# Kernel optimization log

Measured on AMD Instinct MI355X. Metric: run time of the kernel, lower is better.

The kernel has to match this reference:

```python
import jax, jax.numpy as jnp
import numpy as np

B, T, HS, WS = 4, 16, 32, 64          # batch, time, lat, lon
D_MODEL, N_HEADS = 256, 8
E = D_MODEL // N_HEADS                 # 32 per-head dim
MODES = [8, 8, 16]
F_LAST = WS // 2 + 1                   # 33 rfft bins on last dim
M_LAST = MODES[-1]                     # 16 kept rfft bins
M_PANEL = MODES[0] * MODES[1]          # 64 kept (T,HS) panel modes


def _sym_indexes(shape):
    # faithful numpy port of get_symmetry_index_in_fft_pannel
    shape = np.array(shape)
    idx = np.stack([t.flatten() for t in np.meshgrid(*[range(s) for s in shape])])
    idx2 = (-idx) % shape[:, None]
    fftshift = (idx + shape[:, None] // 2) % shape[:, None]
    center = (shape[:, None] - 1) / 2
    order = np.argsort(np.linalg.norm(fftshift - center, axis=0))
    idx = idx[:, order]
    idx2 = idx2[:, order]
    return np.ravel_multi_index(idx, shape), np.ravel_multi_index(idx2, shape)


def _picked_panel():
    # lowest-frequency mode selection honoring Hermitian pairing
    i1, i2 = _sym_indexes((T, HS))
    picked = []
    for a, b in zip(i1, i2):
        if a in picked or b in picked:
            continue
        picked.append(a)
        if len(picked) == M_PANEL:
            break
    return np.array(picked, dtype=np.int32), i1.astype(np.int32), i2.astype(np.int32)


def setup_inputs() -> dict:
    key = jax.random.key(0)
    ks = jax.random.split(key, 12)
    sl = 1.0 / np.float32(np.sqrt(D_MODEL))
    sw = np.float32(0.02)
    panel, s1, s2 = _picked_panel()
    return {
        "x": jax.random.normal(ks[0], (B, T, HS, WS, D_MODEL), jnp.float32),
        "Wq": jax.random.normal(ks[1], (D_MODEL, D_MODEL), jnp.float32) * sl,
        "bq": jnp.zeros((D_MODEL,), jnp.float32),
        "Wk": jax.random.normal(ks[2], (D_MODEL, D_MODEL), jnp.float32) * sl,
        "bk": jnp.zeros((D_MODEL,), jnp.float32),
        "Wv": jax.random.normal(ks[3], (D_MODEL, D_MODEL), jnp.float32) * sl,
        "bv": jnp.zeros((D_MODEL,), jnp.float32),
        "Wo": jax.random.normal(ks[4], (D_MODEL, D_MODEL), jnp.float32) * sl,
        "bo": jnp.zeros((D_MODEL,), jnp.float32),
        "w_real": jax.random.normal(ks[5], (N_HEADS, E, E, M_PANEL, M_LAST), jnp.float32) * sw,
        "w_imag": jax.random.normal(ks[6], (N_HEADS, E, E, M_PANEL, M_LAST), jnp.float32) * sw,
        "panel_idx": jnp.asarray(panel),
        "sym_idx1": jnp.asarray(s1),
        "sym_idx2": jnp.asarray(s2),
    }


def reference(x, Wq, bq, Wk, bk, Wv, bv, Wo, bo, w_real, w_imag,
              panel_idx, sym_idx1, sym_idx2):
    # QKV projections (the torch layer computes all three; FourierBlockN uses q)
    q = (x @ Wq + bq).reshape(B, T, HS, WS, N_HEADS, E).transpose(0, 4, 5, 1, 2, 3)
    _k = (x @ Wk + bk)
    _v = (x @ Wv + bv)
    # rfftn over the spacetime dims -> (B,H,E,T,HS,F_LAST)
    x_ft = jnp.fft.rfftn(q, axes=(-3, -2, -1)).reshape(B, N_HEADS, E, T * HS, F_LAST)
    # gather selected frequency modes
    x_sel = x_ft[:, :, :, panel_idx, :M_LAST]                    # (B,H,E,Mp,Ml)
    w = w_real + 1j * w_imag                                      # (H,E,E,Mp,Ml)
    out_sel = jnp.einsum('bhipf,hiopf->bhopf', x_sel, w)
    out_ft = jnp.zeros_like(x_ft)
    out_ft = out_ft.at[:, :, :, panel_idx, :M_LAST].set(out_sel)
    # canonical_fft_freq: enforce Hermitian symmetry on the (T,HS) panel
    out_ft = out_ft.at[:, :, :, sym_idx1, :].set(
        (out_ft[:, :, :, sym_idx1, :] + jnp.conj(out_ft[:, :, :, sym_idx2, :])) * 0.5)
    out_ft = out_ft.reshape(B, N_HEADS, E, T, HS, F_LAST)
    o = jnp.fft.irfftn(out_ft, s=(T, HS, WS), axes=(-3, -2, -1))  # (B,H,E,T,HS,WS)
    o = o.transpose(0, 3, 4, 5, 1, 2).reshape(B, T, HS, WS, N_HEADS * E)
    return o @ Wo + bo
```

## Files before the change

kernel.cpp:

```cpp
#include <hip/hip_runtime.h>
#include <hip/hip_bf16.h>
#include <cmath>

#define BB 4
#define TT 16
#define HH 32
#define WW 64
#define DD 256
#define NHEAD 8
#define EE 32
#define MP 64
#define ML 16
#define SPAT 32768
#define S2D 512

constexpr size_t OFF_FTRE = 0;
constexpr size_t OFF_FTIM = 1024;
constexpr size_t OFF_FHRE = 2048;
constexpr size_t OFF_FHIM = 4096;
constexpr size_t OFF_CW   = 6144;
constexpr size_t OFF_W64I = 7168;
constexpr size_t OFF_W16  = 9216;
constexpr size_t OFF_FHT  = 9728;
constexpr size_t OFF_GB   = 16384;
constexpr size_t OFF_FW   = OFF_GB + 8388608;
constexpr size_t OFF_X    = OFF_FW + 16777216;
constexpr size_t OFF_V    = OFF_X + 2097152;
constexpr size_t OFF_WT   = OFF_V + 2097152;

typedef short short8 __attribute__((ext_vector_type(8)));
typedef float f32x4 __attribute__((ext_vector_type(4)));

static __device__ __forceinline__ unsigned short f2bf(float x) {
  union { float f; unsigned u; } v; v.f = x;
  unsigned r = v.u + 0x7fffu + ((v.u >> 16) & 1u);
  return (unsigned short)(r >> 16);
}

static __device__ __forceinline__ void gl_lds16(const void* g, void* l) {
  __builtin_amdgcn_global_load_lds((const __attribute__((address_space(1))) void*)g,
                                   (__attribute__((address_space(3))) void*)l, 16, 0, 0);
}

__global__ __launch_bounds__(256) void k0_tables(const int* __restrict__ panel, float* __restrict__ tab) {
  __shared__ int kt[MP], kh[MP];
  int tid = threadIdx.x;
  if (tid < MP) { int s = panel[tid]; kt[tid] = s >> 5; kh[tid] = s & 31; }
  __syncthreads();
  const double PI2 = 6.283185307179586476925286766559;
  for (int i = tid; i < 1024; i += 256) {
    int p = i >> 4, t = i & 15;
    double a = -PI2 * (double)((t * kt[p]) & 15) / 16.0;
    tab[OFF_FTRE + i] = (float)cos(a);
    tab[OFF_FTIM + i] = (float)sin(a);
  }
  for (int i = tid; i < 2048; i += 256) {
    int p = i >> 5, hs = i & 31;
    double a = -PI2 * (double)((hs * kh[p]) & 31) / 32.0;
    tab[OFF_FHRE + i] = (float)cos(a);
    tab[OFF_FHIM + i] = (float)sin(a);
  }
  for (int i = tid; i < 1024; i += 256) {
    int f = i >> 6, wsx = i & 63;
    double a = PI2 * (double)((f * wsx) & 63) / 64.0;
    tab[OFF_CW + i] = (f == 0) ? (1.0f / 64.0f) : (float)(2.0 * cos(a) / 64.0);
  }
  for (int i = tid; i < 2048; i += 256) {
    int wsx = i >> 5, f2 = i & 31; int f = f2 >> 1;
    double a = -PI2 * (double)((wsx * f) & 63) / 64.0;
    tab[OFF_W64I + i] = (f2 & 1) ? (float)sin(a) : (float)cos(a);
  }
  if (tid < 256) {
    int t = tid >> 4, k = tid & 15;
    double a = -PI2 * (double)((t * k) & 15) / 16.0;
    tab[OFF_W16 + 2 * tid]     = (float)cos(a);
    tab[OFF_W16 + 2 * tid + 1] = (float)sin(a);
  }
  for (int i = tid; i < 2048; i += 256) {
    int hs = i >> 6, p = i & 63;
    double a = -PI2 * (double)((hs * kh[p]) & 31) / 32.0;
    tab[OFF_FHT + 2 * i]     = (float)cos(a);
    tab[OFF_FHT + 2 * i + 1] = (float)sin(a);
  }
}

__global__ __launch_bounds__(256) void conv_w(const float* __restrict__ Wq, const float* __restrict__ Wo,
                                              unsigned short* __restrict__ wqt, unsigned short* __restrict__ wot) {
  __shared__ float tile[32][33];
  const float* src = blockIdx.z ? Wo : Wq;
  unsigned short* dst = blockIdx.z ? wot : wqt;
  int k0 = blockIdx.x * 32, d0 = blockIdx.y * 32;
  int tx = threadIdx.x & 31, r4 = threadIdx.x >> 5;
  #pragma unroll
  for (int it = 0; it < 4; it++) {
    int row = r4 + it * 8;
    tile[row][tx] = src[(size_t)(k0 + row) * 256 + d0 + tx];
  }
  __syncthreads();
  #pragma unroll
  for (int it = 0; it < 4; it++) {
    int row = r4 + it * 8;
    dst[(size_t)(d0 + row) * 256 + k0 + tx] = f2bf(tile[tx][row]);
  }
}

__global__ __launch_bounds__(256) void k1f2(const float* __restrict__ x,
                                            const unsigned short* __restrict__ wqt,
                                            const float* __restrict__ bq,
                                            const float* __restrict__ tabp,
                                            float* __restrict__ Fwg) {
  __shared__ char smem[66560];
  char* Asm = smem;
  char* Bl  = smem + 32768;
  float* QL = (float*)(smem + 49152);
  float* WL = (float*)(smem + 58368);
  int b = blockIdx.x >> 9, sg = blockIdx.x & 511;
  int sp0 = sg << 6;
  int tid = threadIdx.x;
  int lane = tid & 63, w = tid >> 6;
  int l15 = lane & 15, kg = lane >> 4;
  int swz = (l15 & 7) << 4;
  for (int i = tid; i < 2048; i += 256) WL[i] = tabp[OFF_W64I + i];
  const float* xbase = x + ((size_t)b * 32768 + sp0) * 256;
  #pragma unroll
  for (int it = 0; it < 8; it++) {
    int fi = it * 2048 + tid * 8;
    int row = fi >> 8, col = fi & 255;
    float4 a4 = *reinterpret_cast<const float4*>(xbase + (size_t)row * 256 + col);
    float4 b4 = *reinterpret_cast<const float4*>(xbase + (size_t)row * 256 + col + 4);
    short8 v;
    v[0] = (short)f2bf(a4.x); v[1] = (short)f2bf(a4.y); v[2] = (short)f2bf(a4.z); v[3] = (short)f2bf(a4.w);
    v[4] = (short)f2bf(b4.x); v[5] = (short)f2bf(b4.y); v[6] = (short)f2bf(b4.z); v[7] = (short)f2bf(b4.w);
    int byteoff = (row * 512 + col * 2) ^ ((row & 7) << 4);
    *reinterpret_cast<short8*>(Asm + byteoff) = v;
  }
  const char* Bbase = (const char*)wqt;
  for (int it8 = 0; it8 < 8; it8++) {
    int d0 = it8 * 32;
    #pragma unroll
    for (int it = 0; it < 4; it++) {
      int o = it * 4096 + tid * 16;
      int row = o >> 9, cb = o & 511;
      gl_lds16(Bbase + (size_t)(d0 + row) * 512 + (cb ^ ((row & 7) << 4)), Bl + o);
    }
    __syncthreads();
    f32x4 acc0 = (f32x4){0.f, 0.f, 0.f, 0.f};
    f32x4 acc1 = (f32x4){0.f, 0.f, 0.f, 0.f};
    #pragma unroll
    for (int ks = 0; ks < 8; ks++) {
      int koff = (ks * 64 + kg * 16) ^ swz;
      short8 af  = *reinterpret_cast<const short8*>(Asm + (w * 16 + l15) * 512 + koff);
      short8 bf0 = *reinterpret_cast<const short8*>(Bl + (size_t)l15 * 512 + koff);
      short8 bf1 = *reinterpret_cast<const short8*>(Bl + (size_t)(16 + l15) * 512 + koff);
      acc0 = __builtin_amdgcn_mfma_f32_16x16x32_bf16(af, bf0, acc0, 0, 0, 0);
      acc1 = __builtin_amdgcn_mfma_f32_16x16x32_bf16(af, bf1, acc1, 0, 0, 0);
    }
    {
      float bq0 = bq[d0 + l15];
      float bq1 = bq[d0 + 16 + l15];
      #pragma unroll
      for (int j = 0; j < 4; j++) {
        QL[(w * 16 + kg * 4 + j) * 36 + l15]      = acc0[j] + bq0;
        QL[(w * 16 + kg * 4 + j) * 36 + 16 + l15] = acc1[j] + bq1;
      }
    }
    __syncthreads();
    {
      int f2q = tid & 7, dd = tid >> 3;
      float r0 = 0.f, r1 = 0.f, r2 = 0.f, r3 = 0.f;
      #pragma unroll 8
      for (int wsx = 0; wsx < 64; wsx++) {
        float q = QL[wsx * 36 + dd];
        float4 wv = *reinterpret_cast<const float4*>(WL + wsx * 32 + f2q * 4);
        r0 += q * wv.x; r1 += q * wv.y; r2 += q * wv.z; r3 += q * wv.w;
      }
      size_t gidx = ((size_t)(b * 512 + sg) * 256 + d0 + dd) * 32 + f2q * 4;
      *reinterpret_cast<float4*>(&Fwg[gidx]) = make_float4(r0, r1, r2, r3);
    }
    __syncthreads();
  }
}

__global__ __launch_bounds__(512) void k3f(const float* __restrict__ Fwg, const float* __restrict__ tabp,
                                           const int* __restrict__ panel, float* __restrict__ X) {
  __shared__ float2 Floc[8192];
  __shared__ float2 fhT[32][64];
  __shared__ float2 W16L[16][16];
  __shared__ int ktl[64];
  int bd = blockIdx.x; int b = bd >> 8; int d = bd & 255;
  int tid = threadIdx.x;
  if (tid < 256) W16L[tid >> 4][tid & 15] = reinterpret_cast<const float2*>(tabp + OFF_W16)[tid];
  for (int i = tid; i < 2048; i += 512) fhT[i >> 6][i & 63] = reinterpret_cast<const float2*>(tabp + OFF_FHT)[i];
  if (tid < 64) ktl[tid] = panel[tid] >> 5;
  {
    const char* gb = (const char*)Fwg;
    #pragma unroll
    for (int r = 0; r < 8; r++) {
      int o = r * 8192 + tid * 16;
      int s = o >> 7; int c16 = (o >> 4) & 7;
      size_t gaddr = ((size_t)(b * 512 + s) * 256 + d) * 128 + (size_t)c16 * 16;
      gl_lds16(gb + gaddr, (char*)Floc + o);
    }
  }
  __syncthreads();
  int hs = tid >> 4, f = tid & 15;
  float2 v[16];
  #pragma unroll
  for (int t = 0; t < 16; t++) v[t] = Floc[(t * 32 + hs) * 16 + f];
  float2 a[16];
  #pragma unroll
  for (int k = 0; k < 16; k++) a[k] = make_float2(0.f, 0.f);
  #pragma unroll
  for (int t = 0; t < 16; t++) {
    float2 vv = v[t];
    #pragma unroll
    for (int k = 0; k < 16; k++) {
      float2 w = W16L[t][k];
      a[k].x += w.x * vv.x - w.y * vv.y;
      a[k].y += w.x * vv.y + w.y * vv.x;
    }
  }
  #pragma unroll
  for (int k = 0; k < 16; k++) Floc[(k * 32 + hs) * 16 + f] = a[k];
  __syncthreads();
  int p2 = tid >> 4;
  float2 res[2];
  #pragma unroll
  for (int half = 0; half < 2; half++) {
    int p = p2 + half * 32;
    int kt = ktl[p];
    float ar = 0.f, ai = 0.f;
    #pragma unroll 8
    for (int h = 0; h < 32; h++) {
      float2 e = fhT[h][p];
      float2 u = Floc[(kt * 32 + h) * 16 + f];
      ar += u.x * e.x - u.y * e.y;
      ai += u.x * e.y + u.y * e.x;
    }
    res[half] = make_float2(ar, ai);
  }
  float2* Xo = reinterpret_cast<float2*>(X) + (size_t)bd * 1024;
  Xo[p2 * 16 + f] = res[0];
  Xo[(p2 + 32) * 16 + f] = res[1];
}

__global__ __launch_bounds__(512) void k3b_mix(const float* __restrict__ X, const float* __restrict__ wreal,
                                               const float* __restrict__ wimag, float* __restrict__ V) {
  __shared__ float2 xs[4][32][16];
  int h = blockIdx.x >> 6;
  int p = blockIdx.x & 63;
  int tid = threadIdx.x;
  const float2* Xv = reinterpret_cast<const float2*>(X);
  for (int i = tid; i < 2048; i += 512) {
    int b = i >> 9, ii = (i >> 4) & 31, f = i & 15;
    xs[b][ii][f] = Xv[((size_t)(b * 256 + h * 32 + ii) * MP + p) * ML + f];
  }
  __syncthreads();
  int o = tid >> 4, f = tid & 15;
  float accr[4] = {0, 0, 0, 0}, acci[4] = {0, 0, 0, 0};
  for (int i = 0; i < 32; i++) {
    size_t wofs = ((((size_t)h * 32 + i) * 32 + o) * MP + p) * ML + f;
    float wr = wreal[wofs], wi = wimag[wofs];
    #pragma unroll
    for (int b = 0; b < 4; b++) {
      float2 xv = xs[b][i][f];
      accr[b] += xv.x * wr - xv.y * wi;
      acci[b] += xv.x * wi + xv.y * wr;
    }
  }
  #pragma unroll
  for (int b = 0; b < 4; b++)
    reinterpret_cast<float2*>(V)[((size_t)(b * 256 + h * 32 + o) * MP + p) * ML + f] =
        make_float2(accr[b], acci[b]);
}

__global__ __launch_bounds__(256) void k4a_inv(const float* __restrict__ V, const float* __restrict__ tabp,
                                               float* __restrict__ gbuf) {
  __shared__ float2 vl[64][16];
  __shared__ float2 ft[64][16];
  __shared__ float2 fh[64][32];
  int bd = blockIdx.x;
  int tid = threadIdx.x;
  const float2* Vv = reinterpret_cast<const float2*>(V) + (size_t)bd * MP * ML;
  for (int i = tid; i < 1024; i += 256) {
    vl[i >> 4][i & 15] = Vv[i];
    ft[i >> 4][i & 15] = make_float2(tabp[OFF_FTRE + i], tabp[OFF_FTIM + i]);
  }
  for (int i = tid; i < 2048; i += 256) fh[i >> 5][i & 31] = make_float2(tabp[OFF_FHRE + i], tabp[OFF_FHIM + i]);
  __syncthreads();
  float g0[16], g1[16];
  #pragma unroll
  for (int f = 0; f < 16; f++) { g0[f] = 0.f; g1[f] = 0.f; }
  int s0 = tid * 2;
  int t0 = s0 >> 5, hs0 = s0 & 31;
  int t1 = (s0 + 1) >> 5, hs1 = (s0 + 1) & 31;
  for (int p = 0; p < 64; p++) {
    float2 et0 = ft[p][t0], eh0 = fh[p][hs0];
    float2 et1 = ft[p][t1], eh1 = fh[p][hs1];
    float er0 = et0.x * eh0.x - et0.y * eh0.y;
    float ei0 = et0.x * eh0.y + et0.y * eh0.x;
    float er1 = et1.x * eh1.x - et1.y * eh1.y;
    float ei1 = et1.x * eh1.y + et1.y * eh1.x;
    #pragma unroll
    for (int f = 0; f < 16; f++) {
      float2 v = vl[p][f];
      g0[f] += v.x * er0 + v.y * ei0;
      g1[f] += v.x * er1 + v.y * ei1;
    }
  }
  float4* gb = reinterpret_cast<float4*>(gbuf + (size_t)bd * 8192 + (size_t)s0 * 16);
  #pragma unroll
  for (int q = 0; q < 4; q++)
    gb[q] = make_float4(g0[q * 4] * (1.f / 512.f), g0[q * 4 + 1] * (1.f / 512.f),
                        g0[q * 4 + 2] * (1.f / 512.f), g0[q * 4 + 3] * (1.f / 512.f));
  #pragma unroll
  for (int q = 0; q < 4; q++)
    gb[4 + q] = make_float4(g1[q * 4] * (1.f / 512.f), g1[q * 4 + 1] * (1.f / 512.f),
                            g1[q * 4 + 2] * (1.f / 512.f), g1[q * 4 + 3] * (1.f / 512.f));
}

__global__ __launch_bounds__(256) void k4b_cos(const float* __restrict__ gbuf, const float* __restrict__ tabp,
                                               unsigned short* __restrict__ ob) {
  __shared__ float Gs[256][17];
  __shared__ float cwL[16][64];
  int s = blockIdx.x, b = blockIdx.y;
  int tid = threadIdx.x;
  for (int i = tid; i < 4096; i += 256) {
    int c = i >> 4, f = i & 15;
    Gs[c][f] = gbuf[(size_t)(b * 256 + c) * 8192 + s * 16 + f];
  }
  for (int i = tid; i < 1024; i += 256) cwL[i >> 6][i & 63] = tabp[OFF_CW + i];
  __syncthreads();
  int c0 = (tid & 63) * 4, wsg = tid >> 6;
  float gv[4][16];
  #pragma unroll
  for (int j = 0; j < 4; j++)
    #pragma unroll
    for (int f = 0; f < 16; f++) gv[j][f] = Gs[c0 + j][f];
  for (int wsi = 0; wsi < 16; wsi++) {
    int wsx = wsg * 16 + wsi;
    float a0 = 0.f, a1 = 0.f, a2 = 0.f, a3 = 0.f;
    #pragma unroll
    for (int f = 0; f < 16; f++) {
      float cwv = cwL[f][wsx];
      a0 += gv[0][f] * cwv; a1 += gv[1][f] * cwv; a2 += gv[2][f] * cwv; a3 += gv[3][f] * cwv;
    }
    ushort4 u;
    u.x = f2bf(a0); u.y = f2bf(a1); u.z = f2bf(a2); u.w = f2bf(a3);
    *reinterpret_cast<ushort4*>(&ob[((size_t)b * SPAT + (size_t)s * 64 + wsx) * 256 + c0]) = u;
  }
}

__global__ __launch_bounds__(256) void k5_mfma(const unsigned short* __restrict__ ob,
                                               const unsigned short* __restrict__ wot,
                                               const float* __restrict__ bo, float* __restrict__ out) {
  __shared__ char smem[34816];
  unsigned short* Al = (unsigned short*)smem;
  unsigned short* Bl = (unsigned short*)(smem + 16384);
  float* OL = (float*)smem;
  int b = blockIdx.x >> 8, sp0 = (blockIdx.x & 255) << 7, d0 = blockIdx.y << 6;
  int tid = threadIdx.x;
  int lane = tid & 63, w = tid >> 6;
  int l15 = lane & 15, kg = lane >> 4;
  int swz = (l15 & 7) << 4;
  f32x4 acc[2][4];
  #pragma unroll
  for (int mi = 0; mi < 2; mi++)
    #pragma unroll
    for (int ni = 0; ni < 4; ni++) acc[mi][ni] = (f32x4){0.f, 0.f, 0.f, 0.f};
  const char* Abase = (const char*)(ob + ((size_t)b * 32768 + sp0) * 256);
  const char* Bbase = (const char*)(wot + (size_t)d0 * 256);
  for (int k0 = 0; k0 < 256; k0 += 64) {
    #pragma unroll
    for (int it = 0; it < 4; it++) {
      int o = tid * 16 + it * 4096;
      int row = o >> 7, cb = o & 127;
      int scb = cb ^ ((row & 7) << 4);
      gl_lds16(Abase + (size_t)row * 512 + k0 * 2 + scb, (char*)Al + o);
    }
    #pragma unroll
    for (int it = 0; it < 2; it++) {
      int o = tid * 16 + it * 4096;
      int row = o >> 7, cb = o & 127;
      int scb = cb ^ ((row & 7) << 4);
      gl_lds16(Bbase + (size_t)row * 512 + k0 * 2 + scb, (char*)Bl + o);
    }
    __syncthreads();
    #pragma unroll
    for (int ks = 0; ks < 2; ks++) {
      int koff = (ks * 64 + kg * 16) ^ swz;
      short8 af[2], bfr[4];
      #pragma unroll
      for (int mi = 0; mi < 2; mi++)
        af[mi] = *(const short8*)((const char*)Al + (w * 32 + mi * 16 + l15) * 128 + koff);
      #pragma unroll
      for (int ni = 0; ni < 4; ni++)
        bfr[ni] = *(const short8*)((const char*)Bl + (ni * 16 + l15) * 128 + koff);
      #pragma unroll
      for (int mi = 0; mi < 2; mi++)
        #pragma unroll
        for (int ni = 0; ni < 4; ni++)
          acc[mi][ni] = __builtin_amdgcn_mfma_f32_16x16x32_bf16(af[mi], bfr[ni], acc[mi][ni], 0, 0, 0);
    }
    __syncthreads();
  }
  #pragma unroll
  for (int ni = 0; ni < 4; ni++) {
    float bov = bo[d0 + ni * 16 + l15];
    #pragma unroll
    for (int mi = 0; mi < 2; mi++) {
      f32x4 v = acc[mi][ni];
      int m = w * 32 + mi * 16 + kg * 4;
      #pragma unroll
      for (int j = 0; j < 4; j++)
        OL[(m + j) * 68 + ni * 16 + l15] = v[j] + bov;
    }
  }
  __syncthreads();
  int f4 = tid & 15, r0 = tid >> 4;
  #pragma unroll
  for (int r = 0; r < 8; r++) {
    int m = r * 16 + r0;
    float4 val = *reinterpret_cast<const float4*>(&OL[m * 68 + f4 * 4]);
    *reinterpret_cast<float4*>(&out[((size_t)b * SPAT + sp0 + m) * 256 + d0 + f4 * 4]) = val;
  }
}

extern "C" void kernel_launch(void* const* d_in, const int* in_sizes, int n_in,
                              void* d_out, int out_size, void* d_ws, size_t ws_size,
                              hipStream_t stream) {
  const float* x  = (const float*)d_in[0];
  const float* Wq = (const float*)d_in[1];
  const float* bq = (const float*)d_in[2];
  const float* Wo = (const float*)d_in[7];
  const float* bo = (const float*)d_in[8];
  const float* wr = (const float*)d_in[9];
  const float* wi = (const float*)d_in[10];
  const int* panel = (const int*)d_in[11];
  float* wsf = (float*)d_ws;
  float* out = (float*)d_out;

  float*          gbuf = wsf + OFF_GB;
  unsigned short* obb  = (unsigned short*)(wsf + OFF_FW);
  unsigned short* wqt  = (unsigned short*)(wsf + OFF_WT);
  unsigned short* wot  = wqt + 65536;

  k0_tables<<<dim3(1), dim3(256), 0, stream>>>(panel, wsf);
  conv_w<<<dim3(8, 8, 2), dim3(256), 0, stream>>>(Wq, Wo, wqt, wot);
  k1f2<<<dim3(2048), dim3(256), 0, stream>>>(x, wqt, bq, wsf, wsf + OFF_FW);
  k3f<<<dim3(1024), dim3(512), 0, stream>>>(wsf + OFF_FW, wsf, panel, wsf + OFF_X);
  k3b_mix<<<dim3(512), dim3(512), 0, stream>>>(wsf + OFF_X, wr, wi, wsf + OFF_V);
  k4a_inv<<<dim3(1024), dim3(256), 0, stream>>>(wsf + OFF_V, wsf, gbuf);
  k4b_cos<<<dim3(512, 4), dim3(256), 0, stream>>>(gbuf, wsf, obb);
  k5_mfma<<<dim3(1024, 4), dim3(256), 0, stream>>>(obb, wot, bo, out);
}
```

Baseline: 370.3 us.

## Load Wq fragments directly from global and batch DFT stage over 128 channels

The k1f2 kernel no longer stages each 32-column Wq tile into LDS with async copies and a barrier. Each lane now reads its B fragments straight from global memory, relying on cache. Projection results for four 32-channel groups are collected in a wider 128-column QL buffer before the width-DFT stage runs, and each thread then computes a 4x4 register tile. This cuts barriers per block from about 24 to about 5 and increases register reuse in the DFT loop. In exchange it uses more LDS (about 73KB), which may lower occupancy, and issues uncoalesced global loads for the weights.

```diff
diff --git a/kernel.cpp b/kernel.cpp
--- a/kernel.cpp
+++ b/kernel.cpp
@@ -109,11 +109,10 @@
                                             const float* __restrict__ bq,
                                             const float* __restrict__ tabp,
                                             float* __restrict__ Fwg) {
-  __shared__ char smem[66560];
-  char* Asm = smem;
-  char* Bl  = smem + 32768;
-  float* QL = (float*)(smem + 49152);
-  float* WL = (float*)(smem + 58368);
+  __shared__ char smem[74752];
+  char*  Asm = smem;
+  float* QL  = (float*)(smem + 32768);
+  float* WL  = (float*)(smem + 66560);
   int b = blockIdx.x >> 9, sg = blockIdx.x & 511;
   int sp0 = sg << 6;
   int tid = threadIdx.x;
@@ -134,24 +133,20 @@
     int byteoff = (row * 512 + col * 2) ^ ((row & 7) << 4);
     *reinterpret_cast<short8*>(Asm + byteoff) = v;
   }
-  const char* Bbase = (const char*)wqt;
+  __syncthreads();
   for (int it8 = 0; it8 < 8; it8++) {
     int d0 = it8 * 32;
-    #pragma unroll
-    for (int it = 0; it < 4; it++) {
-      int o = it * 4096 + tid * 16;
-      int row = o >> 9, cb = o & 511;
-      gl_lds16(Bbase + (size_t)(d0 + row) * 512 + (cb ^ ((row & 7) << 4)), Bl + o);
-    }
-    __syncthreads();
+    int dl = (it8 & 3) * 32;
     f32x4 acc0 = (f32x4){0.f, 0.f, 0.f, 0.f};
     f32x4 acc1 = (f32x4){0.f, 0.f, 0.f, 0.f};
+    const unsigned short* wr0 = wqt + (size_t)(d0 + l15) * 256;
+    const unsigned short* wr1 = wqt + (size_t)(d0 + 16 + l15) * 256;
     #pragma unroll
     for (int ks = 0; ks < 8; ks++) {
       int koff = (ks * 64 + kg * 16) ^ swz;
       short8 af  = *reinterpret_cast<const short8*>(Asm + (w * 16 + l15) * 512 + koff);
-      short8 bf0 = *reinterpret_cast<const short8*>(Bl + (size_t)l15 * 512 + koff);
-      short8 bf1 = *reinterpret_cast<const short8*>(Bl + (size_t)(16 + l15) * 512 + koff);
+      short8 bf0 = *reinterpret_cast<const short8*>(wr0 + ks * 32 + kg * 8);
+      short8 bf1 = *reinterpret_cast<const short8*>(wr1 + ks * 32 + kg * 8);
       acc0 = __builtin_amdgcn_mfma_f32_16x16x32_bf16(af, bf0, acc0, 0, 0, 0);
       acc1 = __builtin_amdgcn_mfma_f32_16x16x32_bf16(af, bf1, acc1, 0, 0, 0);
     }
@@ -160,24 +155,34 @@
       float bq1 = bq[d0 + 16 + l15];
       #pragma unroll
       for (int j = 0; j < 4; j++) {
-        QL[(w * 16 + kg * 4 + j) * 36 + l15]      = acc0[j] + bq0;
-        QL[(w * 16 + kg * 4 + j) * 36 + 16 + l15] = acc1[j] + bq1;
+        QL[(w * 16 + kg * 4 + j) * 132 + dl + l15]      = acc0[j] + bq0;
+        QL[(w * 16 + kg * 4 + j) * 132 + dl + 16 + l15] = acc1[j] + bq1;
       }
     }
-    __syncthreads();
-    {
-      int f2q = tid & 7, dd = tid >> 3;
-      float r0 = 0.f, r1 = 0.f, r2 = 0.f, r3 = 0.f;
+    if ((it8 & 3) == 3) {
+      __syncthreads();
+      int h = it8 >> 2;
+      int dq = tid >> 3, f2h = tid & 7;
+      f32x4 acc[4];
+      acc[0] = (f32x4){0.f, 0.f, 0.f, 0.f};
+      acc[1] = (f32x4){0.f, 0.f, 0.f, 0.f};
+      acc[2] = (f32x4){0.f, 0.f, 0.f, 0.f};
+      acc[3] = (f32x4){0.f, 0.f, 0.f, 0.f};
       #pragma unroll 8
       for (int wsx = 0; wsx < 64; wsx++) {
-        float q = QL[wsx * 36 + dd];
-        float4 wv = *reinterpret_cast<const float4*>(WL + wsx * 32 + f2q * 4);
-        r0 += q * wv.x; r1 += q * wv.y; r2 += q * wv.z; r3 += q * wv.w;
+        f32x4 q  = *reinterpret_cast<const f32x4*>(QL + wsx * 132 + dq * 4);
+        f32x4 wv = *reinterpret_cast<const f32x4*>(WL + wsx * 32 + f2h * 4);
+        acc[0] += wv * q[0];
+        acc[1] += wv * q[1];
+        acc[2] += wv * q[2];
+        acc[3] += wv * q[3];
       }
-      size_t gidx = ((size_t)(b * 512 + sg) * 256 + d0 + dd) * 32 + f2q * 4;
-      *reinterpret_cast<float4*>(&Fwg[gidx]) = make_float4(r0, r1, r2, r3);
-    }
-    __syncthreads();
+      size_t gb = ((size_t)(b * 512 + sg) * 256 + h * 128 + dq * 4) * 32 + f2h * 4;
+      #pragma unroll
+      for (int di = 0; di < 4; di++)
+        *reinterpret_cast<f32x4*>(&Fwg[gb + (size_t)di * 32]) = acc[di];
+      if (it8 < 7) __syncthreads();
+    }
   }
 }
 
```

After: 417.4 us. 1.13x slower.

## Retile Q projection GEMM into 128x64 output tiles with K-loop

Applied to the files above, without the earlier changes.

Restructures the fused Q-projection plus W-axis DFT kernel. The old kernel staged a full 64x256 x-tile in LDS and walked eight 32-column output chunks, with barriers and a DFT pass after each chunk. The new kernel gives each block a 128-row x 64-column output tile, loops over K in chunks of 64, and holds a 2x4 grid of MFMA accumulators per wave. It then runs the DFT once on the whole tile with vectorised LDS reads. This cuts LDS use and barrier count and raises MFMA work per load, but each x row is now read and converted to bf16 by four separate blocks, which relies on L2 hits among neighbouring blocks.

```diff
diff --git a/kernel.cpp b/kernel.cpp
--- a/kernel.cpp
+++ b/kernel.cpp
@@ -104,80 +104,107 @@
   }
 }
 
-__global__ __launch_bounds__(256) void k1f2(const float* __restrict__ x,
+__global__ __launch_bounds__(256) void k1f3(const float* __restrict__ x,
                                             const unsigned short* __restrict__ wqt,
                                             const float* __restrict__ bq,
                                             const float* __restrict__ tabp,
                                             float* __restrict__ Fwg) {
-  __shared__ char smem[66560];
-  char* Asm = smem;
-  char* Bl  = smem + 32768;
-  float* QL = (float*)(smem + 49152);
-  float* WL = (float*)(smem + 58368);
-  int b = blockIdx.x >> 9, sg = blockIdx.x & 511;
-  int sp0 = sg << 6;
+  __shared__ char smem[43008];
+  char*  Al = smem;
+  char*  Bl = smem + 16384;
+  float* QL = (float*)smem;
+  float* WL = (float*)(smem + 34816);
+  int d0 = blockIdx.x << 6;
+  int b = blockIdx.y >> 8, st = blockIdx.y & 255;
+  int sp0 = st << 7;
   int tid = threadIdx.x;
   int lane = tid & 63, w = tid >> 6;
   int l15 = lane & 15, kg = lane >> 4;
   int swz = (l15 & 7) << 4;
   for (int i = tid; i < 2048; i += 256) WL[i] = tabp[OFF_W64I + i];
+  f32x4 acc[2][4];
+  #pragma unroll
+  for (int mi = 0; mi < 2; mi++)
+    #pragma unroll
+    for (int ni = 0; ni < 4; ni++) acc[mi][ni] = (f32x4){0.f, 0.f, 0.f, 0.f};
   const float* xbase = x + ((size_t)b * 32768 + sp0) * 256;
-  #pragma unroll
-  for (int it = 0; it < 8; it++) {
-    int fi = it * 2048 + tid * 8;
-    int row = fi >> 8, col = fi & 255;
-    float4 a4 = *reinterpret_cast<const float4*>(xbase + (size_t)row * 256 + col);
-    float4 b4 = *reinterpret_cast<const float4*>(xbase + (size_t)row * 256 + col + 4);
-    short8 v;
-    v[0] = (short)f2bf(a4.x); v[1] = (short)f2bf(a4.y); v[2] = (short)f2bf(a4.z); v[3] = (short)f2bf(a4.w);
-    v[4] = (short)f2bf(b4.x); v[5] = (short)f2bf(b4.y); v[6] = (short)f2bf(b4.z); v[7] = (short)f2bf(b4.w);
-    int byteoff = (row * 512 + col * 2) ^ ((row & 7) << 4);
-    *reinterpret_cast<short8*>(Asm + byteoff) = v;
-  }
-  const char* Bbase = (const char*)wqt;
-  for (int it8 = 0; it8 < 8; it8++) {
-    int d0 = it8 * 32;
+  const char* Bbase = (const char*)(wqt + (size_t)d0 * 256);
+  for (int k0 = 0; k0 < 256; k0 += 64) {
     #pragma unroll
     for (int it = 0; it < 4; it++) {
+      int idx = it * 256 + tid;
+      int row = idx >> 3, g8 = idx & 7;
+      const float* src = xbase + (size_t)row * 256 + k0 + g8 * 8;
+      float4 a4 = *reinterpret_cast<const float4*>(src);
+      float4 b4 = *reinterpret_cast<const float4*>(src + 4);
+      short8 v;
+      v[0] = (short)f2bf(a4.x); v[1] = (short)f2bf(a4.y); v[2] = (short)f2bf(a4.z); v[3] = (short)f2bf(a4.w);
+      v[4] = (short)f2bf(b4.x); v[5] = (short)f2bf(b4.y); v[6] = (short)f2bf(b4.z); v[7] = (short)f2bf(b4.w);
+      int byteoff = (row * 128 + g8 * 16) ^ ((row & 7) << 4);
+      *reinterpret_cast<short8*>(Al + byteoff) = v;
+    }
+    #pragma unroll
+    for (int it = 0; it < 2; it++) {
       int o = it * 4096 + tid * 16;
-      int row = o >> 9, cb = o & 511;
-      gl_lds16(Bbase + (size_t)(d0 + row) * 512 + (cb ^ ((row & 7) << 4)), Bl + o);
+      int row = o >> 7, cb = o & 127;
+      gl_lds16(Bbase + (size_t)row * 512 + k0 * 2 + (cb ^ ((row & 7) << 4)), Bl + o);
     }
     __syncthreads();
-    f32x4 acc0 = (f32x4){0.f, 0.f, 0.f, 0.f};
-    f32x4 acc1 = (f32x4){0.f, 0.f, 0.f, 0.f};
-    #pragma unroll
-    for (int ks = 0; ks < 8; ks++) {
+    #pragma unroll
+    for (int ks = 0; ks < 2; ks++) {
       int koff = (ks * 64 + kg * 16) ^ swz;
-      short8 af  = *reinterpret_cast<const short8*>(Asm + (w * 16 + l15) * 512 + koff);
-      short8 bf0 = *reinterpret_cast<const short8*>(Bl + (size_t)l15 * 512 + koff);
-      short8 bf1 = *reinterpret_cast<const short8*>(Bl + (size_t)(16 + l15) * 512 + koff);
-      acc0 = __builtin_amdgcn_mfma_f32_16x16x32_bf16(af, bf0, acc0, 0, 0, 0);
-      acc1 = __builtin_amdgcn_mfma_f32_16x16x32_bf16(af, bf1, acc1, 0, 0, 0);
-    }
-    {
-      float bq0 = bq[d0 + l15];
-      float bq1 = bq[d0 + 16 + l15];
-      #pragma unroll
-      for (int j = 0; j < 4; j++) {
-        QL[(w * 16 + kg * 4 + j) * 36 + l15]      = acc0[j] + bq0;
-        QL[(w * 16 + kg * 4 + j) * 36 + 16 + l15] = acc1[j] + bq1;
-      }
+      short8 af[2], bfr[4];
+      #pragma unroll
+      for (int mi = 0; mi < 2; mi++)
+        af[mi] = *reinterpret_cast<const short8*>(Al + (w * 32 + mi * 16 + l15) * 128 + koff);
+      #pragma unroll
+      for (int ni = 0; ni < 4; ni++)
+        bfr[ni] = *reinterpret_cast<const short8*>(Bl + (ni * 16 + l15) * 128 + koff);
+      #pragma unroll
+      for (int mi = 0; mi < 2; mi++)
+        #pragma unroll
+        for (int ni = 0; ni < 4; ni++)
+          acc[mi][ni] = __builtin_amdgcn_mfma_f32_16x16x32_bf16(af[mi], bfr[ni], acc[mi][ni], 0, 0, 0);
     }
     __syncthreads();
-    {
-      int f2q = tid & 7, dd = tid >> 3;
-      float r0 = 0.f, r1 = 0.f, r2 = 0.f, r3 = 0.f;
-      #pragma unroll 8
-      for (int wsx = 0; wsx < 64; wsx++) {
-        float q = QL[wsx * 36 + dd];
-        float4 wv = *reinterpret_cast<const float4*>(WL + wsx * 32 + f2q * 4);
-        r0 += q * wv.x; r1 += q * wv.y; r2 += q * wv.z; r3 += q * wv.w;
-      }
-      size_t gidx = ((size_t)(b * 512 + sg) * 256 + d0 + dd) * 32 + f2q * 4;
-      *reinterpret_cast<float4*>(&Fwg[gidx]) = make_float4(r0, r1, r2, r3);
-    }
-    __syncthreads();
+  }
+  #pragma unroll
+  for (int ni = 0; ni < 4; ni++) {
+    float bqv = bq[d0 + ni * 16 + l15];
+    #pragma unroll
+    for (int mi = 0; mi < 2; mi++) {
+      f32x4 vv = acc[mi][ni];
+      int m = w * 32 + mi * 16 + kg * 4;
+      #pragma unroll
+      for (int j = 0; j < 4; j++)
+        QL[(m + j) * 68 + ni * 16 + l15] = vv[j] + bqv;
+    }
+  }
+  __syncthreads();
+  {
+    int s = tid >> 7, dq = (tid >> 3) & 15, f2q = tid & 7;
+    f32x4 a2[4];
+    a2[0] = (f32x4){0.f, 0.f, 0.f, 0.f};
+    a2[1] = (f32x4){0.f, 0.f, 0.f, 0.f};
+    a2[2] = (f32x4){0.f, 0.f, 0.f, 0.f};
+    a2[3] = (f32x4){0.f, 0.f, 0.f, 0.f};
+    const float* qbase = QL + (s * 64) * 68 + dq * 4;
+    const float* wbase = WL + f2q * 4;
+    #pragma unroll 8
+    for (int wsx = 0; wsx < 64; wsx++) {
+      f32x4 q  = *reinterpret_cast<const f32x4*>(qbase + wsx * 68);
+      f32x4 wv = *reinterpret_cast<const f32x4*>(wbase + wsx * 32);
+      a2[0] += wv * q[0];
+      a2[1] += wv * q[1];
+      a2[2] += wv * q[2];
+      a2[3] += wv * q[3];
+    }
+    int sgl = st * 2 + s;
+    #pragma unroll
+    for (int di = 0; di < 4; di++) {
+      size_t gidx = ((size_t)(b * 512 + sgl) * 256 + d0 + dq * 4 + di) * 32 + f2q * 4;
+      *reinterpret_cast<f32x4*>(&Fwg[gidx]) = a2[di];
+    }
   }
 }
 
@@ -447,7 +474,7 @@
 
   k0_tables<<<dim3(1), dim3(256), 0, stream>>>(panel, wsf);
   conv_w<<<dim3(8, 8, 2), dim3(256), 0, stream>>>(Wq, Wo, wqt, wot);
-  k1f2<<<dim3(2048), dim3(256), 0, stream>>>(x, wqt, bq, wsf, wsf + OFF_FW);
+  k1f3<<<dim3(4, 1024), dim3(256), 0, stream>>>(x, wqt, bq, wsf, wsf + OFF_FW);
   k3f<<<dim3(1024), dim3(512), 0, stream>>>(wsf + OFF_FW, wsf, panel, wsf + OFF_X);
   k3b_mix<<<dim3(512), dim3(512), 0, stream>>>(wsf + OFF_X, wr, wi, wsf + OFF_V);
   k4a_inv<<<dim3(1024), dim3(256), 0, stream>>>(wsf + OFF_V, wsf, gbuf);
```

Result: no change. 367.8 us (-0.7%).
